# Kernel tuning notes

Measured on AMD Instinct MI355X. Metric: run time of the kernel, lower is better.

The kernel has to match this reference:

```python
import jax, jax.numpy as jnp
import numpy as np

EMBED_DIM = 1024
NUM_HEADS = 16
DEPTH = 12
HEAD_DIM = EMBED_DIM // NUM_HEADS // 2  # 32
LAMBDA_INIT = float(0.8 - 0.6 * np.exp(-0.3 * DEPTH))
B, T = 2, 2048


def setup_inputs() -> dict:
    key = jax.random.key(0)
    ks = jax.random.split(key, 10)
    s = 0.02
    return {
        "query": jax.random.normal(ks[0], (B, T, EMBED_DIM), jnp.float32),
        "Wq": jax.random.normal(ks[1], (EMBED_DIM, EMBED_DIM), jnp.float32) * s,
        "Wk": jax.random.normal(ks[2], (EMBED_DIM, EMBED_DIM), jnp.float32) * s,
        "Wv": jax.random.normal(ks[3], (EMBED_DIM, EMBED_DIM), jnp.float32) * s,
        "Wo": jax.random.normal(ks[4], (EMBED_DIM, EMBED_DIM), jnp.float32) * s,
        "lambda_q1": jax.random.normal(ks[5], (HEAD_DIM,), jnp.float32) * 0.1,
        "lambda_k1": jax.random.normal(ks[6], (HEAD_DIM,), jnp.float32) * 0.1,
        "lambda_q2": jax.random.normal(ks[7], (HEAD_DIM,), jnp.float32) * 0.1,
        "lambda_k2": jax.random.normal(ks[8], (HEAD_DIM,), jnp.float32) * 0.1,
        "subln_w": jnp.ones((2 * HEAD_DIM,), jnp.float32),
    }


def reference(query, Wq, Wk, Wv, Wo, lambda_q1, lambda_k1, lambda_q2, lambda_k2, subln_w):
    Bsz, Tt, E = query.shape
    H, hd = NUM_HEADS, HEAD_DIM
    scaling = hd ** -0.5
    # projections (torch Linear: x @ W.T), W stored [out, in]
    q = jnp.einsum('bte,fe->btf', query, Wq).reshape(Bsz, Tt, 2 * H, hd).transpose(0, 2, 1, 3)
    k = jnp.einsum('bse,fe->bsf', query, Wk).reshape(Bsz, Tt, 2 * H, hd).transpose(0, 2, 1, 3)
    v = jnp.einsum('bse,fe->bsf', query, Wv).reshape(Bsz, Tt, H, 2 * hd).transpose(0, 2, 1, 3)
    q = q * scaling
    # dual attention map [B, 2H, T, T], softmax in fp32
    scores = jnp.einsum('bhtd,bhsd->bhts', q, k)
    attn_w = jax.nn.softmax(scores.astype(jnp.float32), axis=-1).astype(q.dtype)
    # learned lambda
    lam1 = jnp.exp(jnp.sum(lambda_q1 * lambda_k1))
    lam2 = jnp.exp(jnp.sum(lambda_q2 * lambda_k2))
    lam = lam1 - lam2 + LAMBDA_INIT
    aw = attn_w.reshape(Bsz, H, 2, Tt, Tt)
    aw = aw[:, :, 0] - lam * aw[:, :, 1]  # [B, H, T, T]
    attn = jnp.einsum('bhts,bhsd->bhtd', aw, v)  # [B, H, T, 2*hd]
    # RMSNorm over last dim (fp32), eps=1e-5, elementwise affine
    x32 = attn.astype(jnp.float32)
    normed = (x32 * jax.lax.rsqrt(jnp.mean(x32 * x32, axis=-1, keepdims=True) + 1e-5)).astype(attn.dtype)
    attn = normed * subln_w
    attn = attn * (1.0 - LAMBDA_INIT)
    out = attn.transpose(0, 2, 1, 3).reshape(Bsz, Tt, H * 2 * hd)
    return jnp.einsum('bte,fe->btf', out, Wo)
```

## Files before the change

kernel.cpp:

```cpp
#include <hip/hip_runtime.h>

typedef short bf16x8 __attribute__((ext_vector_type(8)));
typedef float f32x4 __attribute__((ext_vector_type(4)));
typedef float f32x16 __attribute__((ext_vector_type(16)));
typedef unsigned short ushort_t;
typedef unsigned int uint32;

#define LAMBDA_INIT 0.7836057665316245f
#define TT 2048
#define EE 1024

__device__ __forceinline__ ushort_t f2bf(float x) {
  uint32 b = __float_as_uint(x);
  b += 0x7fffu + ((b >> 16) & 1u);
  return (ushort_t)(b >> 16);
}

__device__ __forceinline__ uint32 cvtpk(float lo, float hi) {
  uint32 r;
  asm("v_cvt_pk_bf16_f32 %0, %1, %2" : "=v"(r) : "v"(lo), "v"(hi));
  return r;
}

__device__ __forceinline__ float fexp2(float x) {
#if __has_builtin(__builtin_amdgcn_exp2f)
  return __builtin_amdgcn_exp2f(x);
#else
  float r;
  asm("v_exp_f32 %0, %1\n\ts_nop 1" : "=v"(r) : "v"(x));
  return r;
#endif
}

__device__ __forceinline__ bf16x8 mkfrag(uint32 a, uint32 b, uint32 c, uint32 d) {
  union { uint32 w[4]; bf16x8 v; } u;
  u.w[0] = a; u.w[1] = b; u.w[2] = c; u.w[3] = d;
  return u.v;
}

__device__ __forceinline__ void gload16(const void* g, void* l) {
  __builtin_amdgcn_global_load_lds(
      (const __attribute__((address_space(1))) uint32*)g,
      (__attribute__((address_space(3))) uint32*)l, 16, 0, 0);
}

__global__ __launch_bounds__(256) void cvt_all(const float* __restrict__ X,
                                               const float* __restrict__ Wq,
                                               const float* __restrict__ Wk,
                                               const float* __restrict__ Wv,
                                               const float* __restrict__ Wo,
                                               ushort_t* __restrict__ out) {
  const int i = blockIdx.x * 256 + threadIdx.x;
  const float* src;
  int off;
  if (i < 1048576)      { src = X;  off = 0; }
  else if (i < 1310720) { src = Wq; off = 1048576; }
  else if (i < 1572864) { src = Wk; off = 1310720; }
  else if (i < 1835008) { src = Wv; off = 1572864; }
  else                  { src = Wo; off = 1835008; }
  const float4 v = reinterpret_cast<const float4*>(src)[i - off];
  ushort4 o;
  o.x = f2bf(v.x); o.y = f2bf(v.y); o.z = f2bf(v.z); o.w = f2bf(v.w);
  reinterpret_cast<ushort4*>(out)[i] = o;
}

template <int MODE>
__global__ __launch_bounds__(256) void gemm_bt(const ushort_t* __restrict__ A,
                                               const ushort_t* __restrict__ B,
                                               void* __restrict__ C,
                                               int M, int N, int K, float scale) {
  __shared__ ushort_t As[128 * 32];
  __shared__ ushort_t Bs[128 * 32];
  const int tid = threadIdx.x;
  const int lane = tid & 63, wid = tid >> 6;
  const int wr = wid >> 1, wc = wid & 1;
  const int r16 = lane & 15, g = lane >> 4;
  const int m0 = blockIdx.x * 128, n0 = blockIdx.y * 128;
  f32x4 acc[4][4] = {};
  for (int k0 = 0; k0 < K; k0 += 32) {
#pragma unroll
    for (int c = 0; c < 2; ++c) {
      int eo = wid * 1024 + c * 512 + lane * 8;
      int row = eo >> 5, col = eo & 31;
      gload16(A + (size_t)(m0 + row) * K + k0 + col, As + wid * 1024 + c * 512);
      gload16(B + (size_t)(n0 + row) * K + k0 + col, Bs + wid * 1024 + c * 512);
    }
    __syncthreads();
    bf16x8 af[4], bfg[4];
#pragma unroll
    for (int m = 0; m < 4; ++m)
      af[m] = *reinterpret_cast<const bf16x8*>(As + (wr * 64 + m * 16 + r16) * 32 + g * 8);
#pragma unroll
    for (int n = 0; n < 4; ++n)
      bfg[n] = *reinterpret_cast<const bf16x8*>(Bs + (wc * 64 + n * 16 + r16) * 32 + g * 8);
#pragma unroll
    for (int m = 0; m < 4; ++m)
#pragma unroll
      for (int n = 0; n < 4; ++n)
        acc[m][n] = __builtin_amdgcn_mfma_f32_16x16x32_bf16(af[m], bfg[n], acc[m][n], 0, 0, 0);
    __syncthreads();
  }
#pragma unroll
  for (int m = 0; m < 4; ++m)
#pragma unroll
    for (int n = 0; n < 4; ++n) {
      if constexpr (MODE == 3) {
        const size_t MN = (size_t)4096 * EE;
        const int col = n0 + wc * 64 + n * 16 + r16;
        const int seg = col >> 10;
        const int cl = col & 1023;
        if (seg == 2) {
          int row0 = m0 + wr * 64 + m * 16 + g * 4;
          int bb = row0 >> 11, t0v = row0 & (TT - 1);
          ushort4 pk;
          pk.x = f2bf(acc[m][n][0]); pk.y = f2bf(acc[m][n][1]);
          pk.z = f2bf(acc[m][n][2]); pk.w = f2bf(acc[m][n][3]);
          *reinterpret_cast<ushort4*>(
              (ushort_t*)C + 2 * MN +
              ((size_t)(bb * 16 + (cl >> 6)) * 64 + (cl & 63)) * TT + t0v) = pk;
        } else {
          const float sc = (seg == 0) ? scale : 1.0f;
          const size_t base = (size_t)seg * MN;
#pragma unroll
          for (int r = 0; r < 4; ++r) {
            int row = m0 + wr * 64 + m * 16 + g * 4 + r;
            ((ushort_t*)C)[base + (size_t)row * EE + cl] = f2bf(acc[m][n][r] * sc);
          }
        }
      } else {
#pragma unroll
        for (int r = 0; r < 4; ++r) {
          int row = m0 + wr * 64 + m * 16 + g * 4 + r;
          int col = n0 + wc * 64 + n * 16 + r16;
          reinterpret_cast<float*>(C)[(size_t)row * N + col] = acc[m][n][r] * scale;
        }
      }
    }
}


#define PHALF(sv, oL, oT0, oT1, vf)                                                     \
  do {                                                                                  \
    float p_[16];                                                                       \
    _Pragma("unroll") for (int i_ = 0; i_ < 16; ++i_) p_[i_] = fexp2(sv[i_]);           \
    auto wA_ = __builtin_amdgcn_permlane32_swap((int)cvtpk(p_[0], p_[1]),               \
                                                (int)cvtpk(p_[4], p_[5]), false, false);\
    auto wB_ = __builtin_amdgcn_permlane32_swap((int)cvtpk(p_[2], p_[3]),               \
                                                (int)cvtpk(p_[6], p_[7]), false, false);\
    auto wC_ = __builtin_amdgcn_permlane32_swap((int)cvtpk(p_[8], p_[9]),               \
                                                (int)cvtpk(p_[12], p_[13]), false, false);\
    auto wD_ = __builtin_amdgcn_permlane32_swap((int)cvtpk(p_[10], p_[11]),             \
                                                (int)cvtpk(p_[14], p_[15]), false, false);\
    bf16x8 pa0_ = mkfrag(wA_[0], wB_[0], wA_[1], wB_[1]);                               \
    bf16x8 pa1_ = mkfrag(wC_[0], wD_[0], wC_[1], wD_[1]);                               \
    oL = __builtin_amdgcn_mfma_f32_32x32x16_bf16(pa0_, onesf, oL, 0, 0, 0);             \
    oL = __builtin_amdgcn_mfma_f32_32x32x16_bf16(pa1_, onesf, oL, 0, 0, 0);             \
    oT0 = __builtin_amdgcn_mfma_f32_32x32x16_bf16(pa0_, vf[0][0], oT0, 0, 0, 0);        \
    oT0 = __builtin_amdgcn_mfma_f32_32x32x16_bf16(pa1_, vf[1][0], oT0, 0, 0, 0);        \
    oT1 = __builtin_amdgcn_mfma_f32_32x32x16_bf16(pa0_, vf[0][1], oT1, 0, 0, 0);        \
    oT1 = __builtin_amdgcn_mfma_f32_32x32x16_bf16(pa1_, vf[1][1], oT1, 0, 0, 0);        \
  } while (0)

#define STAGE(bi, kv0)                                                                  \
  do {                                                                                  \
    gload16(Kg + (size_t)((kv0) + wid * 8 + (lane >> 3)) * EE +                         \
                (((lane & 7) ^ (lane >> 3)) << 3),                                      \
            Ksm[bi] + wid * 512);                                                       \
    gload16(Vg + (size_t)(wid * 16 + (lane >> 2)) * TT + (kv0) +                        \
                ((((lane & 3) ^ ((lane >> 3) & 3)) << 3)),                              \
            Vsm[bi] + wid * 512);                                                       \
  } while (0)

__global__ __launch_bounds__(256, 2) void attn_fused(
    const ushort_t* __restrict__ Q, const ushort_t* __restrict__ K,
    const ushort_t* __restrict__ Vt,
    const float* __restrict__ lq1, const float* __restrict__ lk1,
    const float* __restrict__ lq2, const float* __restrict__ lk2,
    const float* __restrict__ w, ushort_t* __restrict__ X2) {
  __shared__ ushort_t Ksm[2][32 * 64];
  __shared__ ushort_t Vsm[2][64 * 32];
  const int tid = threadIdx.x, lane = tid & 63, wid = tid >> 6;
  const int l31 = lane & 31, hh = lane >> 5;
  const int bid = blockIdx.x;
  const int slice = (bid & 7) + 8 * (bid >> 7);
  const int qb = (bid >> 3) & 15;
  const int bb = slice >> 4, h = slice & 15;
  const int q0 = qb * 128 + wid * 32;

  float prod = (lane < 32) ? lq1[l31] * lk1[l31] : lq2[l31] * lk2[l31];
#pragma unroll
  for (int off = 1; off < 32; off <<= 1) prod += __shfl_xor(prod, off, 32);
  const float lam = __expf(__shfl(prod, 0, 64)) - __expf(__shfl(prod, 32, 64)) + LAMBDA_INIT;

  const ushort_t* Qp = Q + (size_t)(bb * TT + q0 + l31) * EE + h * 64 + hh * 8;
  const bf16x8 qf00 = *reinterpret_cast<const bf16x8*>(Qp);
  const bf16x8 qf01 = *reinterpret_cast<const bf16x8*>(Qp + 16);
  const bf16x8 qf10 = *reinterpret_cast<const bf16x8*>(Qp + 32);
  const bf16x8 qf11 = *reinterpret_cast<const bf16x8*>(Qp + 48);

  const ushort_t* Kg = K + (size_t)bb * TT * EE + h * 64;
  const ushort_t* Vg = Vt + (size_t)(bb * 16 + h) * 64 * TT;
  const int kswz = (l31 & 7) << 3;
  const int vswz = ((l31 >> 1) & 3) << 3;

  const short ONE = (short)0x3F80;
  const bf16x8 onesf = {ONE, ONE, ONE, ONE, ONE, ONE, ONE, ONE};

  f32x16 o00 = {}, o01 = {}, o10 = {}, o11 = {};
  f32x16 oL0 = {}, oL1 = {};

  STAGE(0, 0);
  for (int it = 0; it < TT / 32; ++it) {
    const int cur = it & 1;
    __syncthreads();
    if (it + 1 < TT / 32) STAGE(cur ^ 1, (it + 1) * 32);

    const ushort_t* Kt_ = Ksm[cur];
    const ushort_t* Vt_ = Vsm[cur];
    bf16x8 kf[2][2], vf[2][2];
#pragma unroll
    for (int hf = 0; hf < 2; ++hf)
#pragma unroll
      for (int ks = 0; ks < 2; ++ks)
        kf[hf][ks] = *reinterpret_cast<const bf16x8*>(
            Kt_ + l31 * 64 + ((hf * 32 + ks * 16 + hh * 8) ^ kswz));
#pragma unroll
    for (int ks = 0; ks < 2; ++ks)
#pragma unroll
      for (int dc = 0; dc < 2; ++dc)
        vf[ks][dc] = *reinterpret_cast<const bf16x8*>(
            Vt_ + (dc * 32 + l31) * 32 + ((ks * 16 + hh * 8) ^ vswz));

    __builtin_amdgcn_s_setprio(1);
    const f32x16 zz = {};
    f32x16 s0_ = __builtin_amdgcn_mfma_f32_32x32x16_bf16(kf[0][0], qf00, zz, 0, 0, 0);
    s0_ = __builtin_amdgcn_mfma_f32_32x32x16_bf16(kf[0][1], qf01, s0_, 0, 0, 0);
    f32x16 s1_ = __builtin_amdgcn_mfma_f32_32x32x16_bf16(kf[1][0], qf10, zz, 0, 0, 0);
    s1_ = __builtin_amdgcn_mfma_f32_32x32x16_bf16(kf[1][1], qf11, s1_, 0, 0, 0);
    PHALF(s0_, oL0, o00, o01, vf);
    PHALF(s1_, oL1, o10, o11, vf);
    __builtin_amdgcn_s_setprio(0);
  }

  const float w0v = w[l31];
  const float w1v = w[32 + l31];
#pragma unroll
  for (int r = 0; r < 16; ++r) {
    const int qrel = (r & 3) + 8 * (r >> 2) + 4 * hh;
    const float il0 = 1.0f / oL0[r];
    const float il1 = lam / oL1[r];
    const float x0 = o00[r] * il0 - o10[r] * il1;
    const float x1 = o01[r] * il0 - o11[r] * il1;
    float ss = x0 * x0 + x1 * x1;
#pragma unroll
    for (int off = 1; off < 32; off <<= 1) ss += __shfl_xor(ss, off, 64);
    const float sc = rsqrtf(ss * (1.0f / 64.0f) + 1e-5f) * (1.0f - LAMBDA_INIT);
    const size_t ob = (size_t)(bb * TT + q0 + qrel) * EE + h * 64 + l31;
    X2[ob] = f2bf(x0 * sc * w0v);
    X2[ob + 32] = f2bf(x1 * sc * w1v);
  }
}

extern "C" void kernel_launch(void* const* d_in, const int* in_sizes, int n_in,
                              void* d_out, int out_size, void* d_ws, size_t ws_size,
                              hipStream_t stream) {
  const float* X = (const float*)d_in[0];
  const float* Wq = (const float*)d_in[1];
  const float* Wk = (const float*)d_in[2];
  const float* Wv = (const float*)d_in[3];
  const float* Wo = (const float*)d_in[4];
  const float* lq1 = (const float*)d_in[5];
  const float* lk1 = (const float*)d_in[6];
  const float* lq2 = (const float*)d_in[7];
  const float* lk2 = (const float*)d_in[8];
  const float* slw = (const float*)d_in[9];

  const int M = 4096, E = EE;

  ushort_t* Xb = (ushort_t*)d_ws;
  ushort_t* Wqb = Xb + (size_t)M * E;
  ushort_t* Wob = Wqb + (size_t)3 * E * E;
  ushort_t* Qb = Wob + (size_t)E * E;
  ushort_t* Kb = Qb + (size_t)M * E;
  ushort_t* Vtb = Kb + (size_t)M * E;
  ushort_t* X2 = Vtb + (size_t)M * E;

  cvt_all<<<8192, 256, 0, stream>>>(X, Wq, Wk, Wv, Wo, Xb);

  gemm_bt<3><<<dim3(M / 128, 3072 / 128), 256, 0, stream>>>(
      Xb, Wqb, Qb, M, 3072, E, 0.17677669529663687f * 1.4426950408889634f);

  attn_fused<<<512, 256, 0, stream>>>(Qb, Kb, Vtb, lq1, lk1, lq2, lk2, slw, X2);

  gemm_bt<0><<<dim3(M / 128, E / 128), 256, 0, stream>>>(X2, Wob, d_out, M, E, E, 1.0f);
}
```

Baseline: 139.9 us.

## Split dual-softmax attention into per-half kernels plus separate combine/RMSNorm pass

The fused attention kernel, which handled both softmax maps of a head in one block, is replaced by a kernel that handles a single half-head per block. This doubles the block count to 1024 and raises the occupancy hint to 3. The KV tile grows to 64 keys with a new LDS swizzle. Per-half normalized outputs go to an fp32 workspace, and a new combine_rms kernel applies the lambda subtraction, RMSNorm and scaling. This adds an extra launch and a round-trip of 32 MB of fp32 intermediates, and it depends on the workspace being large enough.

```diff
diff --git a/kernel.cpp b/kernel.cpp
--- a/kernel.cpp
+++ b/kernel.cpp
@@ -26,9 +26,7 @@
 #if __has_builtin(__builtin_amdgcn_exp2f)
   return __builtin_amdgcn_exp2f(x);
 #else
-  float r;
-  asm("v_exp_f32 %0, %1\n\ts_nop 1" : "=v"(r) : "v"(x));
-  return r;
+  return exp2f(x);
 #endif
 }
 
@@ -163,102 +161,116 @@
 
 #define STAGE(bi, kv0)                                                                  \
   do {                                                                                  \
-    gload16(Kg + (size_t)((kv0) + wid * 8 + (lane >> 3)) * EE +                         \
-                (((lane & 7) ^ (lane >> 3)) << 3),                                      \
+    const int g_ = (lane & 7) ^ (lane >> 3);                                            \
+    const int r8_ = lane >> 3;                                                          \
+    gload16(Kg + (size_t)((kv0) + wid * 8 + r8_ + ((g_ >> 2) << 5)) * EE + (g_ & 3) * 8,\
             Ksm[bi] + wid * 512);                                                       \
-    gload16(Vg + (size_t)(wid * 16 + (lane >> 2)) * TT + (kv0) +                        \
-                ((((lane & 3) ^ ((lane >> 3) & 3)) << 3)),                              \
+    gload16(Vg + (size_t)(wid * 8 + r8_) * TT + (kv0) + g_ * 8,                         \
             Vsm[bi] + wid * 512);                                                       \
+    gload16(Vg + (size_t)((wid + 4) * 8 + r8_) * TT + (kv0) + g_ * 8,                   \
+            Vsm[bi] + (wid + 4) * 512);                                                 \
   } while (0)
 
-__global__ __launch_bounds__(256, 2) void attn_fused(
-    const ushort_t* __restrict__ Q, const ushort_t* __restrict__ K,
-    const ushort_t* __restrict__ Vt,
-    const float* __restrict__ lq1, const float* __restrict__ lk1,
-    const float* __restrict__ lq2, const float* __restrict__ lk2,
-    const float* __restrict__ w, ushort_t* __restrict__ X2) {
+__global__ __launch_bounds__(256, 3) void attn_half(const ushort_t* __restrict__ Q,
+                                                    const ushort_t* __restrict__ K,
+                                                    const ushort_t* __restrict__ Vt,
+                                                    float* __restrict__ OH) {
   __shared__ ushort_t Ksm[2][32 * 64];
-  __shared__ ushort_t Vsm[2][64 * 32];
+  __shared__ ushort_t Vsm[2][64 * 64];
   const int tid = threadIdx.x, lane = tid & 63, wid = tid >> 6;
   const int l31 = lane & 31, hh = lane >> 5;
   const int bid = blockIdx.x;
-  const int slice = (bid & 7) + 8 * (bid >> 7);
-  const int qb = (bid >> 3) & 15;
-  const int bb = slice >> 4, h = slice & 15;
+  const int xcd = bid & 7, idx = bid >> 3;
+  const int pair = xcd * 4 + (idx >> 5);
+  const int half = (idx >> 4) & 1, qb = idx & 15;
+  const int bb = pair >> 4;
+  const int h2 = ((pair & 15) << 1) | half;
   const int q0 = qb * 128 + wid * 32;
 
-  float prod = (lane < 32) ? lq1[l31] * lk1[l31] : lq2[l31] * lk2[l31];
-#pragma unroll
-  for (int off = 1; off < 32; off <<= 1) prod += __shfl_xor(prod, off, 32);
-  const float lam = __expf(__shfl(prod, 0, 64)) - __expf(__shfl(prod, 32, 64)) + LAMBDA_INIT;
-
-  const ushort_t* Qp = Q + (size_t)(bb * TT + q0 + l31) * EE + h * 64 + hh * 8;
-  const bf16x8 qf00 = *reinterpret_cast<const bf16x8*>(Qp);
-  const bf16x8 qf01 = *reinterpret_cast<const bf16x8*>(Qp + 16);
-  const bf16x8 qf10 = *reinterpret_cast<const bf16x8*>(Qp + 32);
-  const bf16x8 qf11 = *reinterpret_cast<const bf16x8*>(Qp + 48);
-
-  const ushort_t* Kg = K + (size_t)bb * TT * EE + h * 64;
-  const ushort_t* Vg = Vt + (size_t)(bb * 16 + h) * 64 * TT;
-  const int kswz = (l31 & 7) << 3;
-  const int vswz = ((l31 >> 1) & 3) << 3;
+  const ushort_t* Qp = Q + (size_t)(bb * TT + q0 + l31) * EE + h2 * 32 + hh * 8;
+  const bf16x8 qf0 = *reinterpret_cast<const bf16x8*>(Qp);
+  const bf16x8 qf1 = *reinterpret_cast<const bf16x8*>(Qp + 16);
+
+  const ushort_t* Kg = K + (size_t)bb * TT * EE + h2 * 32;
+  const ushort_t* Vg = Vt + (size_t)(bb * 16 + (h2 >> 1)) * 64 * TT;
+  const int rs = l31 & 7;
 
   const short ONE = (short)0x3F80;
   const bf16x8 onesf = {ONE, ONE, ONE, ONE, ONE, ONE, ONE, ONE};
 
-  f32x16 o00 = {}, o01 = {}, o10 = {}, o11 = {};
-  f32x16 oL0 = {}, oL1 = {};
+  f32x16 o0 = {}, o1 = {}, oL = {};
 
   STAGE(0, 0);
-  for (int it = 0; it < TT / 32; ++it) {
+  for (int it = 0; it < TT / 64; ++it) {
     const int cur = it & 1;
     __syncthreads();
-    if (it + 1 < TT / 32) STAGE(cur ^ 1, (it + 1) * 32);
+    if (it + 1 < TT / 64) STAGE(cur ^ 1, (it + 1) * 64);
 
     const ushort_t* Kt_ = Ksm[cur];
     const ushort_t* Vt_ = Vsm[cur];
-    bf16x8 kf[2][2], vf[2][2];
-#pragma unroll
-    for (int hf = 0; hf < 2; ++hf)
+    __builtin_amdgcn_s_setprio(1);
+#pragma unroll
+    for (int sub = 0; sub < 2; ++sub) {
+      bf16x8 kf0 = *reinterpret_cast<const bf16x8*>(
+          Kt_ + l31 * 64 + (((sub * 4 + hh) ^ rs) << 3));
+      bf16x8 kf1 = *reinterpret_cast<const bf16x8*>(
+          Kt_ + l31 * 64 + (((sub * 4 + 2 + hh) ^ rs) << 3));
+      bf16x8 vf[2][2];
 #pragma unroll
       for (int ks = 0; ks < 2; ++ks)
-        kf[hf][ks] = *reinterpret_cast<const bf16x8*>(
-            Kt_ + l31 * 64 + ((hf * 32 + ks * 16 + hh * 8) ^ kswz));
-#pragma unroll
-    for (int ks = 0; ks < 2; ++ks)
-#pragma unroll
-      for (int dc = 0; dc < 2; ++dc)
-        vf[ks][dc] = *reinterpret_cast<const bf16x8*>(
-            Vt_ + (dc * 32 + l31) * 32 + ((ks * 16 + hh * 8) ^ vswz));
-
-    __builtin_amdgcn_s_setprio(1);
-    const f32x16 zz = {};
-    f32x16 s0_ = __builtin_amdgcn_mfma_f32_32x32x16_bf16(kf[0][0], qf00, zz, 0, 0, 0);
-    s0_ = __builtin_amdgcn_mfma_f32_32x32x16_bf16(kf[0][1], qf01, s0_, 0, 0, 0);
-    f32x16 s1_ = __builtin_amdgcn_mfma_f32_32x32x16_bf16(kf[1][0], qf10, zz, 0, 0, 0);
-    s1_ = __builtin_amdgcn_mfma_f32_32x32x16_bf16(kf[1][1], qf11, s1_, 0, 0, 0);
-    PHALF(s0_, oL0, o00, o01, vf);
-    PHALF(s1_, oL1, o10, o11, vf);
+#pragma unroll
+        for (int dc = 0; dc < 2; ++dc)
+          vf[ks][dc] = *reinterpret_cast<const bf16x8*>(
+              Vt_ + (dc * 32 + l31) * 64 + (((sub * 4 + ks * 2 + hh) ^ rs) << 3));
+      const f32x16 zz = {};
+      f32x16 s_ = __builtin_amdgcn_mfma_f32_32x32x16_bf16(kf0, qf0, zz, 0, 0, 0);
+      s_ = __builtin_amdgcn_mfma_f32_32x32x16_bf16(kf1, qf1, s_, 0, 0, 0);
+      PHALF(s_, oL, o0, o1, vf);
+    }
     __builtin_amdgcn_s_setprio(0);
   }
 
-  const float w0v = w[l31];
-  const float w1v = w[32 + l31];
 #pragma unroll
   for (int r = 0; r < 16; ++r) {
     const int qrel = (r & 3) + 8 * (r >> 2) + 4 * hh;
-    const float il0 = 1.0f / oL0[r];
-    const float il1 = lam / oL1[r];
-    const float x0 = o00[r] * il0 - o10[r] * il1;
-    const float x1 = o01[r] * il0 - o11[r] * il1;
-    float ss = x0 * x0 + x1 * x1;
-#pragma unroll
-    for (int off = 1; off < 32; off <<= 1) ss += __shfl_xor(ss, off, 64);
-    const float sc = rsqrtf(ss * (1.0f / 64.0f) + 1e-5f) * (1.0f - LAMBDA_INIT);
-    const size_t ob = (size_t)(bb * TT + q0 + qrel) * EE + h * 64 + l31;
-    X2[ob] = f2bf(x0 * sc * w0v);
-    X2[ob + 32] = f2bf(x1 * sc * w1v);
+    const float il = 1.0f / oL[r];
+    const size_t base = ((size_t)(bb * 32 + h2) * TT + q0 + qrel) * 64 + l31;
+    OH[base] = o0[r] * il;
+    OH[base + 32] = o1[r] * il;
   }
+}
+
+__global__ __launch_bounds__(256) void combine_rms(const float* __restrict__ O,
+                                                   const float* __restrict__ lq1,
+                                                   const float* __restrict__ lk1,
+                                                   const float* __restrict__ lq2,
+                                                   const float* __restrict__ lk2,
+                                                   const float* __restrict__ w,
+                                                   ushort_t* __restrict__ X2) {
+  const int T = TT;
+  const int lane = threadIdx.x & 63, wid = threadIdx.x >> 6;
+  const int idx = blockIdx.x * 4 + wid;
+  const int t = idx & (T - 1);
+  const int h = (idx >> 11) & 15;
+  const int b = idx >> 15;
+
+  int i = lane & 31;
+  float prod = (lane < 32) ? lq1[i] * lk1[i] : lq2[i] * lk2[i];
+#pragma unroll
+  for (int off = 1; off < 32; off <<= 1) prod += __shfl_xor(prod, off, 32);
+  float d1 = __shfl(prod, 0, 64);
+  float d2 = __shfl(prod, 32, 64);
+  float lam = __expf(d1) - __expf(d2) + LAMBDA_INIT;
+
+  size_t base1 = ((size_t)(b * 32 + 2 * h) * T + t) * 64 + lane;
+  size_t base2 = base1 + (size_t)T * 64;
+  float x = O[base1] - lam * O[base2];
+  float ss = x * x;
+#pragma unroll
+  for (int off = 1; off < 64; off <<= 1) ss += __shfl_xor(ss, off, 64);
+  float rms = rsqrtf(ss * (1.0f / 64.0f) + 1e-5f);
+  float outv = x * rms * w[lane] * (1.0f - LAMBDA_INIT);
+  X2[(size_t)(b * T + t) * 1024 + h * 64 + lane] = f2bf(outv);
 }
 
 extern "C" void kernel_launch(void* const* d_in, const int* in_sizes, int n_in,
@@ -284,13 +296,16 @@
   ushort_t* Kb = Qb + (size_t)M * E;
   ushort_t* Vtb = Kb + (size_t)M * E;
   ushort_t* X2 = Vtb + (size_t)M * E;
+  float* OH = (float*)(X2 + (size_t)M * E);
 
   cvt_all<<<8192, 256, 0, stream>>>(X, Wq, Wk, Wv, Wo, Xb);
 
   gemm_bt<3><<<dim3(M / 128, 3072 / 128), 256, 0, stream>>>(
       Xb, Wqb, Qb, M, 3072, E, 0.17677669529663687f * 1.4426950408889634f);
 
-  attn_fused<<<512, 256, 0, stream>>>(Qb, Kb, Vtb, lq1, lk1, lq2, lk2, slw, X2);
+  attn_half<<<1024, 256, 0, stream>>>(Qb, Kb, Vtb, OH);
+
+  combine_rms<<<2 * 16 * TT / 4, 256, 0, stream>>>(OH, lq1, lk1, lq2, lk2, slw, X2);
 
   gemm_bt<0><<<dim3(M / 128, E / 128), 256, 0, stream>>>(X2, Wob, d_out, M, E, E, 1.0f);
 }
```

New measurement: 155.7 us. 1.11x slower.
